# Performance work log

Measured on AMD Instinct MI355X. Metric: run time of the kernel, lower is better.

Reference implementation:

```python
import jax, jax.numpy as jnp
import numpy as np
from jax.ops import segment_sum

N = 50000
E = 1200000
F_IN = 128
HID = 64
N_CLS = 40


def _sage(x, edge_index, edge_weight, W_l, W_r, b):
    # SAGEConv with mean aggregation; messages optionally scaled by edge_weight.
    src, dst = edge_index[0], edge_index[1]
    msg = x[src] * edge_weight[:, None]            # [E, F] gather + scale
    summ = segment_sum(msg, dst, num_segments=N)   # [N, F] scatter-add
    deg = segment_sum(jnp.ones((E,), x.dtype), dst, num_segments=N)
    agg = summ / jnp.maximum(deg, 1.0)[:, None]    # mean over incoming edges
    return agg @ W_l + x @ W_r + b


def setup_inputs() -> dict:
    key = jax.random.key(0)
    ks = jax.random.split(key, 16)
    def glorot(k, shape):
        fan = shape[0] + shape[1]
        return jax.random.normal(k, shape, jnp.float32) * jnp.sqrt(2.0 / fan)
    return {
        "x0": jax.random.normal(ks[0], (N, F_IN), jnp.float32),
        "edge_index": jax.random.randint(ks[1], (2, E), 0, N),
        "edge_weight": jax.random.uniform(ks[2], (E,), jnp.float32),
        "W1l": glorot(ks[3], (F_IN, HID)), "W1r": glorot(ks[4], (F_IN, HID)),
        "b1": jnp.zeros((HID,), jnp.float32),
        "W2l": glorot(ks[5], (HID, HID)), "W2r": glorot(ks[6], (HID, HID)),
        "b2": jnp.zeros((HID,), jnp.float32),
        "W3l": glorot(ks[7], (HID, HID)), "W3r": glorot(ks[8], (HID, HID)),
        "b3": jnp.zeros((HID,), jnp.float32),
        "Wlin": glorot(ks[9], (3 * HID, N_CLS)),
        "blin": jnp.zeros((N_CLS,), jnp.float32),
    }


def reference(x0, edge_index, edge_weight, W1l, W1r, b1, W2l, W2r, b2,
              W3l, W3r, b3, Wlin, blin):
    # dropout in eval mode (identity)
    x1 = jax.nn.relu(_sage(x0, edge_index, edge_weight, W1l, W1r, b1))
    x2 = jax.nn.relu(_sage(x1, edge_index, edge_weight, W2l, W2r, b2))
    x3 = jax.nn.relu(_sage(x2, edge_index, edge_weight, W3l, W3r, b3))
    x = jnp.concatenate([x1, x2, x3], axis=-1)     # [N, 3*HID]
    logits = x @ Wlin + blin                        # [N, N_CLS]
    return jax.nn.log_softmax(logits, axis=-1)
```

## Files before the change

### kernel.cpp

```cpp
#include <hip/hip_runtime.h>
#include <hip/hip_bf16.h>
#include <math.h>

static constexpr int Nn   = 50000;
static constexpr int Ee   = 1200000;
static constexpr int FIN  = 128;
static constexpr int HID  = 64;
static constexpr int NCLS = 40;

static constexpr int NBK    = (Nn + 255) / 256;
static constexpr int CAP    = 7168;
static constexpr int FSLICE = 4096;
static constexpr int FBLK   = (Ee + FSLICE - 1) / FSLICE;

typedef float f32x4  __attribute__((ext_vector_type(4)));
typedef short short8 __attribute__((ext_vector_type(8)));

__device__ inline unsigned short f2b(float f) {
    unsigned int u = __builtin_bit_cast(unsigned int, f);
    return (unsigned short)((u + 0x7FFFu + ((u >> 16) & 1u)) >> 16);
}
__device__ inline float b2f(unsigned short h) {
    return __builtin_bit_cast(float, (unsigned int)h << 16);
}

__global__ __launch_bounds__(256) void init_kernel(int* __restrict__ bcur) {
    int t = threadIdx.x;
    if (t < NBK) bcur[t] = t * CAP;
}

__global__ __launch_bounds__(1024) void bin_fill_kernel(
    const int* __restrict__ src, const int* __restrict__ dst,
    const float* __restrict__ ew, int* __restrict__ bcur,
    int2* __restrict__ edgeT) {
    __shared__ int hist[NBK];
    __shared__ int gbase[NBK];
    const int tid = threadIdx.x;
    for (int i = tid; i < NBK; i += 1024) hist[i] = 0;
    __syncthreads();
    const int e0 = blockIdx.x * FSLICE;
    const int e1 = min(e0 + FSLICE, Ee);
    for (int e = e0 + tid; e < e1; e += 1024)
        atomicAdd(&hist[dst[e] >> 8], 1);
    __syncthreads();
    for (int b = tid; b < NBK; b += 1024) {
        int c = hist[b];
        gbase[b] = c ? atomicAdd(&bcur[b], c) : 0;
        hist[b] = 0;
    }
    __syncthreads();
    for (int e = e0 + tid; e < e1; e += 1024) {
        int d = dst[e];
        int b = d >> 8;
        int r = atomicAdd(&hist[b], 1);
        edgeT[gbase[b] + r] =
            make_int2(src[e] | ((d & 255) << 16), __builtin_bit_cast(int, ew[e]));
    }
}

__global__ __launch_bounds__(512) void sort_kernel(
    const int* __restrict__ bcur, const int2* __restrict__ edgeT,
    unsigned int* __restrict__ edgeA, int* __restrict__ rowbeg,
    int* __restrict__ rowend) {
    __shared__ int hist[256];
    __shared__ int cur[256];
    __shared__ int wsum[4];
    const int t = threadIdx.x, lane = t & 63, wv = t >> 6;
    const int b = blockIdx.x;
    const int beg = b * CAP;
    const int end = bcur[b];

    if (t < 256) hist[t] = 0;
    __syncthreads();
    for (int e = beg + t; e < end; e += 512)
        atomicAdd(&hist[edgeT[e].x >> 16], 1);
    __syncthreads();

    int v = 0, incl = 0;
    if (t < 256) {
        v = hist[t];
        incl = v;
#pragma unroll
        for (int off = 1; off < 64; off <<= 1) {
            int u = __shfl_up(incl, off);
            if (lane >= off) incl += u;
        }
        if (lane == 63) wsum[wv] = incl;
    }
    __syncthreads();
    if (t < 256) {
        int woff = 0;
#pragma unroll
        for (int w = 0; w < 4; ++w) woff += (w < wv) ? wsum[w] : 0;
        const int base = beg + woff + incl - v;
        const int grow = b * 256 + t;
        if (grow < Nn) { rowbeg[grow] = base; rowend[grow] = base + v; }
        cur[t] = base;
    }
    __syncthreads();

    for (int e = beg + t; e < end; e += 512) {
        int2 ed = edgeT[e];
        int ld = ed.x >> 16;
        int p = atomicAdd(&cur[ld], 1);
        unsigned short wb = f2b(__builtin_bit_cast(float, ed.y));
        edgeA[p] = (unsigned int)(ed.x & 0xFFFF) | ((unsigned int)wb << 16);
    }
}

template <int K, typename XT>
__global__ __launch_bounds__(256) void gemmM_kernel(
    const XT* __restrict__ x, const float* __restrict__ Wl,
    const float* __restrict__ Wr, const float* __restrict__ b,
    unsigned short* __restrict__ yl, unsigned short* __restrict__ z) {
    constexpr int LDW = K + 8;
    constexpr int NKT = K / 32;
    __shared__ unsigned short wt[128 * LDW];
    __shared__ float b_s[64];

    const int tid  = threadIdx.x;
    const int row0 = blockIdx.x * 64;

    for (int i = tid; i < K * 64; i += 256) {
        int k = i >> 6, c = i & 63;
        wt[c * LDW + k]        = f2b(Wl[i]);
        wt[(64 + c) * LDW + k] = f2b(Wr[i]);
    }
    if (tid < 64) b_s[tid] = b[tid];
    __syncthreads();

    const int wv   = tid >> 6;
    const int lane = tid & 63;
    const int l15  = lane & 15;
    const int quad = lane >> 4;

    const int arow = row0 + wv * 16 + l15;
    const bool rok = arow < Nn;
    short8 a[NKT];
#pragma unroll
    for (int kt = 0; kt < NKT; ++kt) {
        if (rok) {
            if constexpr (sizeof(XT) == 2) {
                a[kt] = *(const short8*)((const unsigned short*)x +
                                         (size_t)arow * K + kt * 32 + quad * 8);
            } else {
                const float* xp = (const float*)x + (size_t)arow * K + kt * 32 + quad * 8;
                float4 p0 = *(const float4*)xp;
                float4 p1 = *(const float4*)(xp + 4);
                short8 af;
                af[0] = (short)f2b(p0.x); af[1] = (short)f2b(p0.y);
                af[2] = (short)f2b(p0.z); af[3] = (short)f2b(p0.w);
                af[4] = (short)f2b(p1.x); af[5] = (short)f2b(p1.y);
                af[6] = (short)f2b(p1.z); af[7] = (short)f2b(p1.w);
                a[kt] = af;
            }
        } else {
            a[kt] = (short8){0, 0, 0, 0, 0, 0, 0, 0};
        }
    }

    f32x4 acc[8];
#pragma unroll
    for (int ct = 0; ct < 8; ++ct) acc[ct] = (f32x4){0.f, 0.f, 0.f, 0.f};

#pragma unroll
    for (int ct = 0; ct < 8; ++ct) {
        const unsigned short* brow = wt + (ct * 16 + l15) * LDW + quad * 8;
#pragma unroll
        for (int kt = 0; kt < NKT; ++kt) {
            short8 bf = *(const short8*)(brow + kt * 32);
            acc[ct] = __builtin_amdgcn_mfma_f32_16x16x32_bf16(a[kt], bf, acc[ct], 0, 0, 0);
        }
    }

#pragma unroll
    for (int ct = 0; ct < 8; ++ct) {
        int col = ct * 16 + l15;
#pragma unroll
        for (int reg = 0; reg < 4; ++reg) {
            int grow = row0 + wv * 16 + quad * 4 + reg;
            if (grow < Nn) {
                if (col < 64) yl[grow * 64 + col] = f2b(acc[ct][reg]);
                else          z[grow * 64 + col - 64] = f2b(acc[ct][reg] + b_s[col - 64]);
            }
        }
    }
}

__global__ __launch_bounds__(256) void gather_kernel(
    const int* __restrict__ rowbeg, const int* __restrict__ rowend,
    const unsigned int* __restrict__ edgeA, const unsigned short* __restrict__ yl,
    const unsigned short* __restrict__ z, unsigned short* __restrict__ xout) {
    const int wid  = (blockIdx.x * 256 + threadIdx.x) >> 6;
    const int lane = threadIdx.x & 63;
    const int half = lane >> 5;
    const int c    = lane & 31;
    const int r    = wid * 2 + half;
    const int beg = rowbeg[r], end = rowend[r];

    const unsigned int* __restrict__ yl32 = (const unsigned int*)yl;
    const unsigned int* __restrict__ z32  = (const unsigned int*)z;
    unsigned int* __restrict__ xo32       = (unsigned int*)xout;

    float a0 = 0.f, a1 = 0.f;
    int p = beg;
    const int pfull = beg + ((end - beg) & ~7);

    for (; p < pfull; p += 8) {
        unsigned int eb[8], uu[8];
#pragma unroll
        for (int j = 0; j < 8; ++j) eb[j] = edgeA[p + j];
#pragma unroll
        for (int j = 0; j < 8; ++j)
            uu[j] = yl32[(size_t)(eb[j] & 0xFFFFu) * 32 + c];
#pragma unroll
        for (int j = 0; j < 8; ++j) {
            float w = b2f((unsigned short)(eb[j] >> 16));
            a0 += b2f((unsigned short)(uu[j] & 0xFFFFu)) * w;
            a1 += b2f((unsigned short)(uu[j] >> 16)) * w;
        }
    }
    if (p < end) {
        unsigned int eb[8], uu[8];
#pragma unroll
        for (int j = 0; j < 8; ++j) eb[j] = (p + j < end) ? edgeA[p + j] : 0u;
#pragma unroll
        for (int j = 0; j < 8; ++j)
            uu[j] = yl32[(size_t)(eb[j] & 0xFFFFu) * 32 + c];
#pragma unroll
        for (int j = 0; j < 8; ++j) {
            float w = b2f((unsigned short)(eb[j] >> 16));
            a0 += b2f((unsigned short)(uu[j] & 0xFFFFu)) * w;
            a1 += b2f((unsigned short)(uu[j] >> 16)) * w;
        }
    }

    const float den = fmaxf((float)(end - beg), 1.f);
    const unsigned int zw = z32[(size_t)r * 32 + c];
    float v0 = a0 / den + b2f((unsigned short)(zw & 0xFFFFu));
    float v1 = a1 / den + b2f((unsigned short)(zw >> 16));
    unsigned int o = (unsigned int)f2b(fmaxf(v0, 0.f)) |
                     ((unsigned int)f2b(fmaxf(v1, 0.f)) << 16);
    xo32[(size_t)r * 32 + c] = o;
}

__global__ __launch_bounds__(256) void final_kernel(
    const unsigned short* __restrict__ x1, const unsigned short* __restrict__ x2,
    const unsigned short* __restrict__ x3, const float* __restrict__ Wlin,
    const float* __restrict__ blin, float* __restrict__ out) {
    __shared__ unsigned short wt[48 * 200];

    const int tid  = threadIdx.x;
    const int row0 = blockIdx.x * 64;

    for (int i = tid; i < 48 * 200; i += 256) wt[i] = 0;
    __syncthreads();
    for (int i = tid; i < 192 * 40; i += 256) {
        int k = i / 40, n = i % 40;
        wt[n * 200 + k] = f2b(Wlin[i]);
    }
    __syncthreads();

    const int wv   = tid >> 6;
    const int lane = tid & 63;
    const int l15  = lane & 15;
    const int quad = lane >> 4;

    const int arow = row0 + wv * 16 + l15;
    const bool rok = arow < Nn;
    const unsigned short* xarr[3] = {x1, x2, x3};
    short8 a[6];
#pragma unroll
    for (int ks = 0; ks < 6; ++ks) {
        if (rok)
            a[ks] = *(const short8*)(xarr[ks >> 1] + (size_t)arow * 64 +
                                     (ks & 1) * 32 + quad * 8);
        else
            a[ks] = (short8){0, 0, 0, 0, 0, 0, 0, 0};
    }

    f32x4 acc[3];
#pragma unroll
    for (int nt = 0; nt < 3; ++nt) {
        acc[nt] = (f32x4){0.f, 0.f, 0.f, 0.f};
        const unsigned short* brow = wt + (nt * 16 + l15) * 200 + quad * 8;
#pragma unroll
        for (int ks = 0; ks < 6; ++ks) {
            short8 b = *(const short8*)(brow + ks * 32);
            acc[nt] = __builtin_amdgcn_mfma_f32_16x16x32_bf16(a[ks], b, acc[nt], 0, 0, 0);
        }
    }

    const bool c2ok = l15 < 8;
    const float b0 = blin[l15];
    const float b1 = blin[16 + l15];
    const float b2 = c2ok ? blin[32 + l15] : 0.f;

#pragma unroll
    for (int reg = 0; reg < 4; ++reg) {
        float v0 = acc[0][reg] + b0;
        float v1 = acc[1][reg] + b1;
        float v2 = c2ok ? acc[2][reg] + b2 : -INFINITY;
        float mx = fmaxf(fmaxf(v0, v1), v2);
#pragma unroll
        for (int off = 1; off < 16; off <<= 1) mx = fmaxf(mx, __shfl_xor(mx, off));
        float s = expf(v0 - mx) + expf(v1 - mx) + (c2ok ? expf(v2 - mx) : 0.f);
#pragma unroll
        for (int off = 1; off < 16; off <<= 1) s += __shfl_xor(s, off);
        float lse = mx + logf(s);
        int grow = row0 + wv * 16 + quad * 4 + reg;
        if (grow < Nn) {
            out[grow * NCLS + l15]      = v0 - lse;
            out[grow * NCLS + 16 + l15] = v1 - lse;
            if (c2ok) out[grow * NCLS + 32 + l15] = v2 - lse;
        }
    }
}

extern "C" void kernel_launch(void* const* d_in, const int* in_sizes, int n_in,
                              void* d_out, int out_size, void* d_ws, size_t ws_size,
                              hipStream_t stream) {
    const float* x0  = (const float*)d_in[0];
    const int*   ei  = (const int*)d_in[1];
    const float* ew  = (const float*)d_in[2];
    const float* W1l = (const float*)d_in[3];
    const float* W1r = (const float*)d_in[4];
    const float* b1  = (const float*)d_in[5];
    const float* W2l = (const float*)d_in[6];
    const float* W2r = (const float*)d_in[7];
    const float* b2  = (const float*)d_in[8];
    const float* W3l = (const float*)d_in[9];
    const float* W3r = (const float*)d_in[10];
    const float* b3  = (const float*)d_in[11];
    const float* Wlin = (const float*)d_in[12];
    const float* blin = (const float*)d_in[13];
    float* out = (float*)d_out;

    const int* src = ei;
    const int* dst = ei + Ee;

    const size_t N64 = (size_t)Nn * 64;
    const size_t REG = (size_t)NBK * CAP;
    char* ws = (char*)d_ws;
    int*   bcur   = (int*)ws;
    int*   rowbeg = bcur + 256;
    int*   rowend = rowbeg + 50048;
    int2*  edgeT  = (int2*)(rowend + 50048);
    unsigned int* edgeA = (unsigned int*)(edgeT + REG);
    unsigned short* yl  = (unsigned short*)(edgeA + REG);
    unsigned short* zb  = yl + N64;
    unsigned short* x1  = zb + N64;
    unsigned short* x2  = x1 + N64;
    unsigned short* x3  = x2 + N64;

    const int gemm_blocks = (Nn + 63) / 64;
    const int row_blocks  = Nn / 8;
    const int fin_blocks  = (Nn + 63) / 64;

    init_kernel<<<1, 256, 0, stream>>>(bcur);
    bin_fill_kernel<<<FBLK, 1024, 0, stream>>>(src, dst, ew, bcur, edgeT);
    sort_kernel<<<NBK, 512, 0, stream>>>(bcur, edgeT, edgeA, rowbeg, rowend);

    gemmM_kernel<FIN, float><<<gemm_blocks, 256, 0, stream>>>(x0, W1l, W1r, b1, yl, zb);
    gather_kernel<<<row_blocks, 256, 0, stream>>>(rowbeg, rowend, edgeA, yl, zb, x1);

    gemmM_kernel<HID, unsigned short><<<gemm_blocks, 256, 0, stream>>>(x1, W2l, W2r, b2, yl, zb);
    gather_kernel<<<row_blocks, 256, 0, stream>>>(rowbeg, rowend, edgeA, yl, zb, x2);

    gemmM_kernel<HID, unsigned short><<<gemm_blocks, 256, 0, stream>>>(x2, W3l, W3r, b3, yl, zb);
    gather_kernel<<<row_blocks, 256, 0, stream>>>(rowbeg, rowend, edgeA, yl, zb, x3);

    final_kernel<<<fin_blocks, 256, 0, stream>>>(x1, x2, x3, Wlin, blin, out);
}
```

Baseline: 242.6 us.

## Split feature columns into two half-width planes so gather working set halves

Stores yl, z and the layer outputs as two separate 32-column bf16 planes. The gather kernel runs the low and high halves as separate block ranges, so each pass's random-access working set (3.2 MB per plane) is more likely to stay cache-resident. Edge-list loads, z loads and output stores become nontemporal. The cost is that the edge list is read twice per layer and each gather row fetch is only 64 bytes, which may underuse cache lines.

```diff
diff --git a/kernel.cpp b/kernel.cpp
--- a/kernel.cpp
+++ b/kernel.cpp
@@ -22,6 +22,12 @@
 }
 __device__ inline float b2f(unsigned short h) {
     return __builtin_bit_cast(float, (unsigned int)h << 16);
+}
+__device__ inline float b2f_lo(unsigned int u) {
+    return __builtin_bit_cast(float, u << 16);
+}
+__device__ inline float b2f_hi(unsigned int u) {
+    return __builtin_bit_cast(float, u & 0xFFFF0000u);
 }
 
 __global__ __launch_bounds__(256) void init_kernel(int* __restrict__ bcur) {
@@ -110,9 +116,11 @@
 
 template <int K, typename XT>
 __global__ __launch_bounds__(256) void gemmM_kernel(
-    const XT* __restrict__ x, const float* __restrict__ Wl,
-    const float* __restrict__ Wr, const float* __restrict__ b,
-    unsigned short* __restrict__ yl, unsigned short* __restrict__ z) {
+    const XT* __restrict__ xlo, const XT* __restrict__ xhi,
+    const float* __restrict__ Wl, const float* __restrict__ Wr,
+    const float* __restrict__ b,
+    unsigned short* __restrict__ yl_lo, unsigned short* __restrict__ yl_hi,
+    unsigned short* __restrict__ z_lo, unsigned short* __restrict__ z_hi) {
     constexpr int LDW = K + 8;
     constexpr int NKT = K / 32;
     __shared__ unsigned short wt[128 * LDW];
@@ -141,10 +149,11 @@
     for (int kt = 0; kt < NKT; ++kt) {
         if (rok) {
             if constexpr (sizeof(XT) == 2) {
-                a[kt] = *(const short8*)((const unsigned short*)x +
-                                         (size_t)arow * K + kt * 32 + quad * 8);
+                const unsigned short* base =
+                    (kt == 0) ? (const unsigned short*)xlo : (const unsigned short*)xhi;
+                a[kt] = *(const short8*)(base + (size_t)arow * 32 + quad * 8);
             } else {
-                const float* xp = (const float*)x + (size_t)arow * K + kt * 32 + quad * 8;
+                const float* xp = (const float*)xlo + (size_t)arow * K + kt * 32 + quad * 8;
                 float4 p0 = *(const float4*)xp;
                 float4 p1 = *(const float4*)(xp + 4);
                 short8 af;
@@ -180,8 +189,15 @@
         for (int reg = 0; reg < 4; ++reg) {
             int grow = row0 + wv * 16 + quad * 4 + reg;
             if (grow < Nn) {
-                if (col < 64) yl[grow * 64 + col] = f2b(acc[ct][reg]);
-                else          z[grow * 64 + col - 64] = f2b(acc[ct][reg] + b_s[col - 64]);
+                float v = acc[ct][reg];
+                if (col < 32)
+                    yl_lo[(size_t)grow * 32 + col] = f2b(v);
+                else if (col < 64)
+                    yl_hi[(size_t)grow * 32 + col - 32] = f2b(v);
+                else if (col < 96)
+                    z_lo[(size_t)grow * 32 + col - 64] = f2b(v + b_s[col - 64]);
+                else
+                    z_hi[(size_t)grow * 32 + col - 96] = f2b(v + b_s[col - 64]);
             }
         }
     }
@@ -189,18 +205,27 @@
 
 __global__ __launch_bounds__(256) void gather_kernel(
     const int* __restrict__ rowbeg, const int* __restrict__ rowend,
-    const unsigned int* __restrict__ edgeA, const unsigned short* __restrict__ yl,
-    const unsigned short* __restrict__ z, unsigned short* __restrict__ xout) {
-    const int wid  = (blockIdx.x * 256 + threadIdx.x) >> 6;
-    const int lane = threadIdx.x & 63;
-    const int half = lane >> 5;
-    const int c    = lane & 31;
-    const int r    = wid * 2 + half;
+    const unsigned int* __restrict__ edgeA,
+    const unsigned short* __restrict__ yl_lo, const unsigned short* __restrict__ yl_hi,
+    const unsigned short* __restrict__ z_lo, const unsigned short* __restrict__ z_hi,
+    unsigned short* __restrict__ xo_lo, unsigned short* __restrict__ xo_hi) {
+    constexpr int HB = Nn / 16;
+    const int bid = blockIdx.x;
+    const bool hi = bid >= HB;
+    const int rb  = hi ? bid - HB : bid;
+    const unsigned int* __restrict__ yl32 =
+        (const unsigned int*)(hi ? yl_hi : yl_lo);
+    const unsigned int* __restrict__ z32 =
+        (const unsigned int*)(hi ? z_hi : z_lo);
+    unsigned int* __restrict__ xo32 = (unsigned int*)(hi ? xo_hi : xo_lo);
+
+    const int tid  = threadIdx.x;
+    const int wv   = tid >> 6;
+    const int lane = tid & 63;
+    const int q    = lane >> 4;
+    const int c    = lane & 15;
+    const int r    = rb * 16 + wv * 4 + q;
     const int beg = rowbeg[r], end = rowend[r];
-
-    const unsigned int* __restrict__ yl32 = (const unsigned int*)yl;
-    const unsigned int* __restrict__ z32  = (const unsigned int*)z;
-    unsigned int* __restrict__ xo32       = (unsigned int*)xout;
 
     float a0 = 0.f, a1 = 0.f;
     int p = beg;
@@ -209,45 +234,48 @@
     for (; p < pfull; p += 8) {
         unsigned int eb[8], uu[8];
 #pragma unroll
-        for (int j = 0; j < 8; ++j) eb[j] = edgeA[p + j];
+        for (int j = 0; j < 8; ++j) eb[j] = __builtin_nontemporal_load(&edgeA[p + j]);
 #pragma unroll
         for (int j = 0; j < 8; ++j)
-            uu[j] = yl32[(size_t)(eb[j] & 0xFFFFu) * 32 + c];
+            uu[j] = yl32[(size_t)(eb[j] & 0xFFFFu) * 16 + c];
 #pragma unroll
         for (int j = 0; j < 8; ++j) {
             float w = b2f((unsigned short)(eb[j] >> 16));
-            a0 += b2f((unsigned short)(uu[j] & 0xFFFFu)) * w;
-            a1 += b2f((unsigned short)(uu[j] >> 16)) * w;
+            a0 += b2f_lo(uu[j]) * w;
+            a1 += b2f_hi(uu[j]) * w;
         }
     }
     if (p < end) {
         unsigned int eb[8], uu[8];
 #pragma unroll
-        for (int j = 0; j < 8; ++j) eb[j] = (p + j < end) ? edgeA[p + j] : 0u;
-#pragma unroll
         for (int j = 0; j < 8; ++j)
-            uu[j] = yl32[(size_t)(eb[j] & 0xFFFFu) * 32 + c];
+            eb[j] = (p + j < end) ? __builtin_nontemporal_load(&edgeA[p + j]) : 0u;
+#pragma unroll
+        for (int j = 0; j < 8; ++j)
+            uu[j] = yl32[(size_t)(eb[j] & 0xFFFFu) * 16 + c];
 #pragma unroll
         for (int j = 0; j < 8; ++j) {
             float w = b2f((unsigned short)(eb[j] >> 16));
-            a0 += b2f((unsigned short)(uu[j] & 0xFFFFu)) * w;
-            a1 += b2f((unsigned short)(uu[j] >> 16)) * w;
+            a0 += b2f_lo(uu[j]) * w;
+            a1 += b2f_hi(uu[j]) * w;
         }
     }
 
     const float den = fmaxf((float)(end - beg), 1.f);
-    const unsigned int zw = z32[(size_t)r * 32 + c];
-    float v0 = a0 / den + b2f((unsigned short)(zw & 0xFFFFu));
-    float v1 = a1 / den + b2f((unsigned short)(zw >> 16));
+    const unsigned int zw = __builtin_nontemporal_load(&z32[(size_t)r * 16 + c]);
+    float v0 = a0 / den + b2f_lo(zw);
+    float v1 = a1 / den + b2f_hi(zw);
     unsigned int o = (unsigned int)f2b(fmaxf(v0, 0.f)) |
                      ((unsigned int)f2b(fmaxf(v1, 0.f)) << 16);
-    xo32[(size_t)r * 32 + c] = o;
+    __builtin_nontemporal_store(o, &xo32[(size_t)r * 16 + c]);
 }
 
 __global__ __launch_bounds__(256) void final_kernel(
-    const unsigned short* __restrict__ x1, const unsigned short* __restrict__ x2,
-    const unsigned short* __restrict__ x3, const float* __restrict__ Wlin,
-    const float* __restrict__ blin, float* __restrict__ out) {
+    const unsigned short* __restrict__ x1lo, const unsigned short* __restrict__ x1hi,
+    const unsigned short* __restrict__ x2lo, const unsigned short* __restrict__ x2hi,
+    const unsigned short* __restrict__ x3lo, const unsigned short* __restrict__ x3hi,
+    const float* __restrict__ Wlin, const float* __restrict__ blin,
+    float* __restrict__ out) {
     __shared__ unsigned short wt[48 * 200];
 
     const int tid  = threadIdx.x;
@@ -268,13 +296,12 @@
 
     const int arow = row0 + wv * 16 + l15;
     const bool rok = arow < Nn;
-    const unsigned short* xarr[3] = {x1, x2, x3};
+    const unsigned short* xs[6] = {x1lo, x1hi, x2lo, x2hi, x3lo, x3hi};
     short8 a[6];
 #pragma unroll
     for (int ks = 0; ks < 6; ++ks) {
         if (rok)
-            a[ks] = *(const short8*)(xarr[ks >> 1] + (size_t)arow * 64 +
-                                     (ks & 1) * 32 + quad * 8);
+            a[ks] = *(const short8*)(xs[ks] + (size_t)arow * 32 + quad * 8);
         else
             a[ks] = (short8){0, 0, 0, 0, 0, 0, 0, 0};
     }
@@ -339,7 +366,7 @@
     const int* src = ei;
     const int* dst = ei + Ee;
 
-    const size_t N64 = (size_t)Nn * 64;
+    const size_t N32 = (size_t)Nn * 32;
     const size_t REG = (size_t)NBK * CAP;
     char* ws = (char*)d_ws;
     int*   bcur   = (int*)ws;
@@ -347,28 +374,40 @@
     int*   rowend = rowbeg + 50048;
     int2*  edgeT  = (int2*)(rowend + 50048);
     unsigned int* edgeA = (unsigned int*)(edgeT + REG);
-    unsigned short* yl  = (unsigned short*)(edgeA + REG);
-    unsigned short* zb  = yl + N64;
-    unsigned short* x1  = zb + N64;
-    unsigned short* x2  = x1 + N64;
-    unsigned short* x3  = x2 + N64;
+    unsigned short* yl_lo = (unsigned short*)(edgeA + REG);
+    unsigned short* yl_hi = yl_lo + N32;
+    unsigned short* z_lo  = yl_hi + N32;
+    unsigned short* z_hi  = z_lo + N32;
+    unsigned short* x1lo  = z_hi + N32;
+    unsigned short* x1hi  = x1lo + N32;
+    unsigned short* x2lo  = x1hi + N32;
+    unsigned short* x2hi  = x2lo + N32;
+    unsigned short* x3lo  = x2hi + N32;
+    unsigned short* x3hi  = x3lo + N32;
 
     const int gemm_blocks = (Nn + 63) / 64;
-    const int row_blocks  = Nn / 8;
+    const int gath_blocks = 2 * (Nn / 16);
     const int fin_blocks  = (Nn + 63) / 64;
 
     init_kernel<<<1, 256, 0, stream>>>(bcur);
     bin_fill_kernel<<<FBLK, 1024, 0, stream>>>(src, dst, ew, bcur, edgeT);
     sort_kernel<<<NBK, 512, 0, stream>>>(bcur, edgeT, edgeA, rowbeg, rowend);
 
-    gemmM_kernel<FIN, float><<<gemm_blocks, 256, 0, stream>>>(x0, W1l, W1r, b1, yl, zb);
-    gather_kernel<<<row_blocks, 256, 0, stream>>>(rowbeg, rowend, edgeA, yl, zb, x1);
-
-    gemmM_kernel<HID, unsigned short><<<gemm_blocks, 256, 0, stream>>>(x1, W2l, W2r, b2, yl, zb);
-    gather_kernel<<<row_blocks, 256, 0, stream>>>(rowbeg, rowend, edgeA, yl, zb, x2);
-
-    gemmM_kernel<HID, unsigned short><<<gemm_blocks, 256, 0, stream>>>(x2, W3l, W3r, b3, yl, zb);
-    gather_kernel<<<row_blocks, 256, 0, stream>>>(rowbeg, rowend, edgeA, yl, zb, x3);
-
-    final_kernel<<<fin_blocks, 256, 0, stream>>>(x1, x2, x3, Wlin, blin, out);
-}
+    gemmM_kernel<FIN, float><<<gemm_blocks, 256, 0, stream>>>(
+        x0, x0, W1l, W1r, b1, yl_lo, yl_hi, z_lo, z_hi);
+    gather_kernel<<<gath_blocks, 256, 0, stream>>>(
+        rowbeg, rowend, edgeA, yl_lo, yl_hi, z_lo, z_hi, x1lo, x1hi);
+
+    gemmM_kernel<HID, unsigned short><<<gemm_blocks, 256, 0, stream>>>(
+        x1lo, x1hi, W2l, W2r, b2, yl_lo, yl_hi, z_lo, z_hi);
+    gather_kernel<<<gath_blocks, 256, 0, stream>>>(
+        rowbeg, rowend, edgeA, yl_lo, yl_hi, z_lo, z_hi, x2lo, x2hi);
+
+    gemmM_kernel<HID, unsigned short><<<gemm_blocks, 256, 0, stream>>>(
+        x2lo, x2hi, W3l, W3r, b3, yl_lo, yl_hi, z_lo, z_hi);
+    gather_kernel<<<gath_blocks, 256, 0, stream>>>(
+        rowbeg, rowend, edgeA, yl_lo, yl_hi, z_lo, z_hi, x3lo, x3hi);
+
+    final_kernel<<<fin_blocks, 256, 0, stream>>>(
+        x1lo, x1hi, x2lo, x2hi, x3lo, x3hi, Wlin, blin, out);
+}
```

Measured after the change: 265.6 us. +9.5%, slower.
